# Optimization experiments

Hardware: AMD Instinct MI355X
Metric: run time of the kernel (lower is better)

The kernel has to match this reference:

```python
import jax, jax.numpy as jnp
import numpy as np

T, B, I, H, O = 256, 64, 512, 1024, 256


def setup_inputs() -> dict:
    key = jax.random.key(0)
    ks = jax.random.split(key, 7)
    s_ih = 1.0 / np.sqrt(H)
    return {
        "x": jax.random.normal(ks[0], (T, B, I), dtype=jnp.float32),
        "W_ih": jax.random.uniform(ks[1], (4 * H, I), dtype=jnp.float32, minval=-s_ih, maxval=s_ih),
        "W_hh": jax.random.uniform(ks[2], (4 * H, H), dtype=jnp.float32, minval=-s_ih, maxval=s_ih),
        "b_ih": jax.random.uniform(ks[3], (4 * H,), dtype=jnp.float32, minval=-s_ih, maxval=s_ih),
        "b_hh": jax.random.uniform(ks[4], (4 * H,), dtype=jnp.float32, minval=-s_ih, maxval=s_ih),
        "fc_W": jax.random.uniform(ks[5], (O, H), dtype=jnp.float32, minval=-s_ih, maxval=s_ih),
        "fc_b": jax.random.uniform(ks[6], (O,), dtype=jnp.float32, minval=-s_ih, maxval=s_ih),
    }


def _lstm(x, W_ih, W_hh, b_ih, b_hh):
    # x: (T, B, I) seq-first, as PyTorch default. Gate order: i, f, g, o.
    Bsz = x.shape[1]
    Hh = W_hh.shape[1]
    # precompute input projections for all time steps: (T, B, 4H)
    xz = jnp.einsum('tbi,gi->tbg', x, W_ih) + b_ih + b_hh

    def step(carry, xz_t):
        h, c = carry
        z = xz_t + h @ W_hh.T  # (B, 4H)
        i, f, g, o = jnp.split(z, 4, axis=-1)
        i = jax.nn.sigmoid(i)
        f = jax.nn.sigmoid(f)
        g = jnp.tanh(g)
        o = jax.nn.sigmoid(o)
        c = f * c + i * g
        h = o * jnp.tanh(c)
        return (h, c), h

    h0 = jnp.zeros((Bsz, Hh), dtype=x.dtype)
    c0 = jnp.zeros((Bsz, Hh), dtype=x.dtype)
    _, hs = jax.lax.scan(step, (h0, c0), xz)
    return hs  # (T, B, H)


def reference(x, W_ih, W_hh, b_ih, b_hh, fc_W, fc_b):
    out = _lstm(x, W_ih, W_hh, b_ih, b_hh)  # (T, B, H)
    # Faithful to original: out[:, -1, :] indexes the LAST BATCH element
    # (seq-first layout), giving (T, H), then fc -> (T, O).
    last = out[:, -1, :]
    return last @ fc_W.T + fc_b
```

## Files before the change

kernel.cpp:

```cpp
#include <hip/hip_runtime.h>
#include <hip/hip_bf16.h>
#include <stdint.h>

#define T_STEPS 256
#define BATCH   64
#define IN_DIM  512
#define HID     1024
#define OUT_DIM 256
#define G4      4096
#define SENT32  0x7FC07FC0u
#define SENT64  0x7FC07FC07FC07FC0ULL

__device__ __forceinline__ float bfbits2f(uint32_t b16) {
    return __uint_as_float(b16 << 16);
}
__device__ __forceinline__ uint32_t f2bfbits(float f) {
    uint32_t u = __float_as_uint(f);
    u += 0x7fffu + ((u >> 16) & 1u);
    return u >> 16;
}
__device__ __forceinline__ float fast_sigmoid(float x) {
    return 1.f / (1.f + __expf(-x));
}
__device__ __forceinline__ float fast_tanh(float x) {
    return 2.f / (1.f + __expf(-2.f * x)) - 1.f;
}
__device__ __forceinline__ bool any_sent(uint64_t v) {
    uint64_t x = v ^ SENT64;
    return (((x - 0x0001000100010001ULL) & ~x) & 0x8000800080008000ULL) != 0ULL;
}
__device__ __forceinline__ uint64_t poll_load(const uint64_t* p) {
    return __hip_atomic_load(p, __ATOMIC_RELAXED, __HIP_MEMORY_SCOPE_AGENT);
}

__global__ void init_sent(uint32_t* __restrict__ p, int n) {
    int i = blockIdx.x * 256 + threadIdx.x;
    if (i < n) p[i] = SENT32;
}

template<bool ABF16>
__global__ __launch_bounds__(256) void gemm_bt(
    const void* __restrict__ Av, long lda,
    const float* __restrict__ Bw, int ldb,
    const float* __restrict__ bias1,
    float* __restrict__ C, int ldc, int K)
{
    __shared__ float a_lds[64][68];
    __shared__ float w_lds[64][65];
    const int tid = threadIdx.x;
    const int m0 = blockIdx.y * 64, n0 = blockIdx.x * 64;
    const int kl = tid & 63, grp = tid >> 6;
    const int cc = tid & 31, r0 = (tid >> 5) * 8;

    float acc[16];
#pragma unroll
    for (int i = 0; i < 16; ++i) acc[i] = 0.f;

    for (int k0 = 0; k0 < K; k0 += 64) {
        __syncthreads();
#pragma unroll
        for (int i = 0; i < 16; ++i) {
            int r = grp + 4 * i;
            long ai = (long)(m0 + r) * lda + k0 + kl;
            float av = ABF16 ? bfbits2f(((const uint16_t*)Av)[ai])
                             : ((const float*)Av)[ai];
            a_lds[kl][r] = av;
            w_lds[kl][r] = Bw[(long)(n0 + r) * ldb + k0 + kl];
        }
        __syncthreads();
#pragma unroll 16
        for (int k = 0; k < 64; ++k) {
            float4 A0 = *(const float4*)&a_lds[k][r0];
            float4 A1 = *(const float4*)&a_lds[k][r0 + 4];
            float w0 = w_lds[k][cc], w1 = w_lds[k][cc + 32];
            float a[8] = {A0.x, A0.y, A0.z, A0.w, A1.x, A1.y, A1.z, A1.w};
#pragma unroll
            for (int i = 0; i < 8; ++i) {
                acc[i]     += a[i] * w0;
                acc[8 + i] += a[i] * w1;
            }
        }
    }
    float b0 = bias1[n0 + cc], b1 = bias1[n0 + cc + 32];
#pragma unroll
    for (int i = 0; i < 8; ++i) {
        C[(long)(m0 + r0 + i) * ldc + n0 + cc]      = acc[i]     + b0;
        C[(long)(m0 + r0 + i) * ldc + n0 + cc + 32] = acc[8 + i] + b1;
    }
}

#define GROWX(RR) ((long)((RR) >> 3) * HID + 8 * g + ((RR) & 7))

#define WINIT(I) { const int ch_ = ((I) + kpart) & 15; \
    w##I = *(const float4*)(W_hh + wbase + ch_ * 4); }

#define MACS(I) { const float4 hv_ = *(const float4*)(hb + hoff + (((I) + kpart) & 15) * 4); \
    a0 = fmaf(w##I.x, hv_.x, a0); a1 = fmaf(w##I.y, hv_.y, a1); \
    a2 = fmaf(w##I.z, hv_.z, a2); a3 = fmaf(w##I.w, hv_.w, a3); }

__global__ __launch_bounds__(512, 2) void lstm_rec(
    const float* __restrict__ W_hh,
    const float* __restrict__ x,
    const float* __restrict__ W_ih,
    const float* __restrict__ b_ih,
    const float* __restrict__ b_hh,
    uint64_t* __restrict__ h_all)
{
    __shared__ float h_lds[2][HID];
    __shared__ float xz_lds[32][T_STEPS + 1];
    __shared__ float z_lds[32];
    extern __shared__ float dyn_pad[];

    const int g   = blockIdx.x;
    const int tid = threadIdx.x;

    {
        const int wv = tid >> 6;
        const int ln = tid & 63;
        const int rr0 = 4 * wv;
        const long gr0 = GROWX(rr0), gr1 = GROWX(rr0 + 1),
                   gr2 = GROWX(rr0 + 2), gr3 = GROWX(rr0 + 3);
        const float4 p0a = *(const float4*)(W_ih + gr0 * IN_DIM + 8 * ln);
        const float4 p0b = *(const float4*)(W_ih + gr0 * IN_DIM + 8 * ln + 4);
        const float4 p1a = *(const float4*)(W_ih + gr1 * IN_DIM + 8 * ln);
        const float4 p1b = *(const float4*)(W_ih + gr1 * IN_DIM + 8 * ln + 4);
        const float4 p2a = *(const float4*)(W_ih + gr2 * IN_DIM + 8 * ln);
        const float4 p2b = *(const float4*)(W_ih + gr2 * IN_DIM + 8 * ln + 4);
        const float4 p3a = *(const float4*)(W_ih + gr3 * IN_DIM + 8 * ln);
        const float4 p3b = *(const float4*)(W_ih + gr3 * IN_DIM + 8 * ln + 4);
        const float bs0 = b_ih[gr0] + b_hh[gr0];
        const float bs1 = b_ih[gr1] + b_hh[gr1];
        const float bs2 = b_ih[gr2] + b_hh[gr2];
        const float bs3 = b_ih[gr3] + b_hh[gr3];
        for (int t = 0; t < T_STEPS; ++t) {
            const float* xp = x + ((long)t * BATCH + 63) * IN_DIM + 8 * ln;
            const float4 xa = *(const float4*)xp;
            const float4 xb = *(const float4*)(xp + 4);
            float s0 = xa.x*p0a.x + xa.y*p0a.y + xa.z*p0a.z + xa.w*p0a.w
                     + xb.x*p0b.x + xb.y*p0b.y + xb.z*p0b.z + xb.w*p0b.w;
            float s1 = xa.x*p1a.x + xa.y*p1a.y + xa.z*p1a.z + xa.w*p1a.w
                     + xb.x*p1b.x + xb.y*p1b.y + xb.z*p1b.z + xb.w*p1b.w;
            float s2 = xa.x*p2a.x + xa.y*p2a.y + xa.z*p2a.z + xa.w*p2a.w
                     + xb.x*p2b.x + xb.y*p2b.y + xb.z*p2b.z + xb.w*p2b.w;
            float s3 = xa.x*p3a.x + xa.y*p3a.y + xa.z*p3a.z + xa.w*p3a.w
                     + xb.x*p3b.x + xb.y*p3b.y + xb.z*p3b.z + xb.w*p3b.w;
#pragma unroll
            for (int d = 1; d < 64; d <<= 1) {
                s0 += __shfl_xor(s0, d, 64);
                s1 += __shfl_xor(s1, d, 64);
                s2 += __shfl_xor(s2, d, 64);
                s3 += __shfl_xor(s3, d, 64);
            }
            if (ln == 0) {
                xz_lds[rr0 + 0][t] = s0 + bs0;
                xz_lds[rr0 + 1][t] = s1 + bs1;
                xz_lds[rr0 + 2][t] = s2 + bs2;
                xz_lds[rr0 + 3][t] = s3 + bs3;
            }
        }
    }

    if (tid < 256) {
        float4 z4 = {0.f, 0.f, 0.f, 0.f};
        *(float4*)&h_lds[0][4 * tid] = z4;
    }

    const int kpart = tid & 15;
    const int row   = tid >> 4;
    const long grow  = GROWX(row);
    const long wbase = grow * HID + kpart * 64;
    const int  hoff  = kpart * 64;
    float4 w0, w1, w2, w3, w4, w5, w6, w7, w8, w9, w10, w11, w12, w13, w14, w15;
    WINIT(0)  WINIT(1)  WINIT(2)  WINIT(3)
    WINIT(4)  WINIT(5)  WINIT(6)  WINIT(7)
    WINIT(8)  WINIT(9)  WINIT(10) WINIT(11)
    WINIT(12) WINIT(13) WINIT(14) WINIT(15)

    __syncthreads();

    float c_state = 0.f;
    float xz_next = xz_lds[row][0];

    for (int t = 0; t < T_STEPS; ++t) {
        float* hb = h_lds[t & 1];
        if (t > 0 && tid < 128) {
            const uint64_t* src = h_all + (size_t)(t - 1) * 256 + 2 * tid;
            uint64_t v0 = poll_load(src), v1 = poll_load(src + 1);
            if (any_sent(v0) | any_sent(v1)) {
                uint64_t a0_ = poll_load(src), a1_ = poll_load(src + 1);
                uint64_t b0_ = poll_load(src), b1_ = poll_load(src + 1);
                for (;;) {
                    uint64_t c0_ = poll_load(src), c1_ = poll_load(src + 1);
                    if (!(any_sent(v0) | any_sent(v1))) break;
                    v0 = a0_; v1 = a1_;
                    a0_ = b0_; a1_ = b1_;
                    b0_ = c0_; b1_ = c1_;
                }
            }
            float4 f0 = { bfbits2f((uint32_t)( v0        & 0xFFFFu)),
                          bfbits2f((uint32_t)((v0 >> 16) & 0xFFFFu)),
                          bfbits2f((uint32_t)((v0 >> 32) & 0xFFFFu)),
                          bfbits2f((uint32_t)((v0 >> 48) & 0xFFFFu)) };
            float4 f1 = { bfbits2f((uint32_t)( v1        & 0xFFFFu)),
                          bfbits2f((uint32_t)((v1 >> 16) & 0xFFFFu)),
                          bfbits2f((uint32_t)((v1 >> 32) & 0xFFFFu)),
                          bfbits2f((uint32_t)((v1 >> 48) & 0xFFFFu)) };
            *(float4*)&hb[8 * tid]     = f0;
            *(float4*)&hb[8 * tid + 4] = f1;
        }
        __syncthreads();

        const float xz_cur = xz_next;
        const int tn = (t + 1 < T_STEPS) ? t + 1 : t;
        xz_next = xz_lds[row][tn];

        float a0 = 0.f, a1 = 0.f, a2 = 0.f, a3 = 0.f;
        MACS(0)  MACS(1)  MACS(2)  MACS(3)
        MACS(4)  MACS(5)  MACS(6)  MACS(7)
        MACS(8)  MACS(9)  MACS(10) MACS(11)
        MACS(12) MACS(13) MACS(14) MACS(15)
        float sum = (a0 + a1) + (a2 + a3);
        sum += __shfl_xor(sum, 1, 16);
        sum += __shfl_xor(sum, 2, 16);
        sum += __shfl_xor(sum, 4, 16);
        sum += __shfl_xor(sum, 8, 16);
        if (kpart == 0) z_lds[row] = sum + xz_cur;
        __syncthreads();

        if (tid < 8) {
            const float zi = z_lds[tid],      zf = z_lds[8 + tid];
            const float zg = z_lds[16 + tid], zo = z_lds[24 + tid];
            const float ii = fast_sigmoid(zi);
            const float ff = fast_sigmoid(zf);
            const float gg = fast_tanh(zg);
            const float oo = fast_sigmoid(zo);
            c_state = ff * c_state + ii * gg;
            const float h = oo * fast_tanh(c_state);
            uint32_t hbv = f2bfbits(h);
            uint32_t lo  = hbv | (__shfl_down(hbv, 1, 64) << 16);
            uint64_t A = (uint64_t)lo | ((uint64_t)__shfl(lo, 2, 64) << 32);
            uint64_t B = (uint64_t)__shfl(lo, 4, 64)
                       | ((uint64_t)__shfl(lo, 6, 64) << 32);
            if (tid == 0) {
                uint64_t* dst = h_all + (size_t)t * 256 + 2 * g;
                __hip_atomic_store(dst,     A, __ATOMIC_RELAXED, __HIP_MEMORY_SCOPE_AGENT);
                __hip_atomic_store(dst + 1, B, __ATOMIC_RELAXED, __HIP_MEMORY_SCOPE_AGENT);
            }
        }
    }
    (void)dyn_pad;
}

extern "C" void kernel_launch(void* const* d_in, const int* in_sizes, int n_in,
                              void* d_out, int out_size, void* d_ws, size_t ws_size,
                              hipStream_t stream) {
    const float* x    = (const float*)d_in[0];
    const float* W_ih = (const float*)d_in[1];
    const float* W_hh = (const float*)d_in[2];
    const float* b_ih = (const float*)d_in[3];
    const float* b_hh = (const float*)d_in[4];
    const float* fc_W = (const float*)d_in[5];
    const float* fc_b = (const float*)d_in[6];
    float* out = (float*)d_out;

    uint64_t* h_all = (uint64_t*)d_ws;

    init_sent<<<512, 256, 0, stream>>>((uint32_t*)h_all, T_STEPS * HID / 2);

    lstm_rec<<<128, 512, 41984, stream>>>(W_hh, x, W_ih, b_ih, b_hh, h_all);

    gemm_bt<true><<<dim3(OUT_DIM / 64, T_STEPS / 64), 256, 0, stream>>>(
        (const void*)h_all, HID, fc_W, HID, fc_b, out, OUT_DIM, HID);
}
```

Baseline: 1.142 ms.

## Split LSTM recurrence over 256 blocks with W_hh slices held in LDS

Doubles the number of persistent recurrence blocks from 128 to 256, each owning 4 hidden units (16 gate rows) instead of 8. Each block's W_hh slice moves from registers into padded shared memory, and every thread now polls one 64-bit h chunk per step. The aim is to halve per-block matmul work on the serial critical path and spread the work over more CUs. In exchange, every step now reads weights from LDS, and twice as many blocks must synchronise through global-memory polling, which adds sync traffic and latency.

```diff
diff --git a/kernel.cpp b/kernel.cpp
--- a/kernel.cpp
+++ b/kernel.cpp
@@ -10,6 +10,7 @@
 #define G4      4096
 #define SENT32  0x7FC07FC0u
 #define SENT64  0x7FC07FC07FC07FC0ULL
+#define WSTRIDE 1028
 
 __device__ __forceinline__ float bfbits2f(uint32_t b16) {
     return __uint_as_float(b16 << 16);
@@ -89,16 +90,9 @@
     }
 }
 
-#define GROWX(RR) ((long)((RR) >> 3) * HID + 8 * g + ((RR) & 7))
-
-#define WINIT(I) { const int ch_ = ((I) + kpart) & 15; \
-    w##I = *(const float4*)(W_hh + wbase + ch_ * 4); }
-
-#define MACS(I) { const float4 hv_ = *(const float4*)(hb + hoff + (((I) + kpart) & 15) * 4); \
-    a0 = fmaf(w##I.x, hv_.x, a0); a1 = fmaf(w##I.y, hv_.y, a1); \
-    a2 = fmaf(w##I.z, hv_.z, a2); a3 = fmaf(w##I.w, hv_.w, a3); }
-
-__global__ __launch_bounds__(512, 2) void lstm_rec(
+#define GROWX(RR) ((long)((RR) >> 2) * HID + 4 * g + ((RR) & 3))
+
+__global__ __launch_bounds__(256, 1) void lstm_rec(
     const float* __restrict__ W_hh,
     const float* __restrict__ x,
     const float* __restrict__ W_ih,
@@ -106,13 +100,25 @@
     const float* __restrict__ b_hh,
     uint64_t* __restrict__ h_all)
 {
+    __shared__ float W_lds[16][WSTRIDE];
     __shared__ float h_lds[2][HID];
-    __shared__ float xz_lds[32][T_STEPS + 1];
-    __shared__ float z_lds[32];
-    extern __shared__ float dyn_pad[];
+    __shared__ float xz_lds[16][T_STEPS + 1];
+    __shared__ float z_lds[16];
 
     const int g   = blockIdx.x;
     const int tid = threadIdx.x;
+    const int kpart = tid & 15;
+    const int row   = tid >> 4;
+    const long grow = GROWX(row);
+
+    {
+        const float* wsrc = W_hh + grow * HID;
+#pragma unroll
+        for (int i = 0; i < 16; ++i) {
+            const int col = kpart * 64 + ((i + kpart) & 15) * 4;
+            *(float4*)&W_lds[row][col] = *(const float4*)(wsrc + col);
+        }
+    }
 
     {
         const int wv = tid >> 6;
@@ -160,22 +166,10 @@
         }
     }
 
-    if (tid < 256) {
+    {
         float4 z4 = {0.f, 0.f, 0.f, 0.f};
         *(float4*)&h_lds[0][4 * tid] = z4;
     }
-
-    const int kpart = tid & 15;
-    const int row   = tid >> 4;
-    const long grow  = GROWX(row);
-    const long wbase = grow * HID + kpart * 64;
-    const int  hoff  = kpart * 64;
-    float4 w0, w1, w2, w3, w4, w5, w6, w7, w8, w9, w10, w11, w12, w13, w14, w15;
-    WINIT(0)  WINIT(1)  WINIT(2)  WINIT(3)
-    WINIT(4)  WINIT(5)  WINIT(6)  WINIT(7)
-    WINIT(8)  WINIT(9)  WINIT(10) WINIT(11)
-    WINIT(12) WINIT(13) WINIT(14) WINIT(15)
-
     __syncthreads();
 
     float c_state = 0.f;
@@ -183,42 +177,38 @@
 
     for (int t = 0; t < T_STEPS; ++t) {
         float* hb = h_lds[t & 1];
-        if (t > 0 && tid < 128) {
-            const uint64_t* src = h_all + (size_t)(t - 1) * 256 + 2 * tid;
-            uint64_t v0 = poll_load(src), v1 = poll_load(src + 1);
-            if (any_sent(v0) | any_sent(v1)) {
-                uint64_t a0_ = poll_load(src), a1_ = poll_load(src + 1);
-                uint64_t b0_ = poll_load(src), b1_ = poll_load(src + 1);
-                for (;;) {
-                    uint64_t c0_ = poll_load(src), c1_ = poll_load(src + 1);
-                    if (!(any_sent(v0) | any_sent(v1))) break;
-                    v0 = a0_; v1 = a1_;
-                    a0_ = b0_; a1_ = b1_;
-                    b0_ = c0_; b1_ = c1_;
-                }
-            }
-            float4 f0 = { bfbits2f((uint32_t)( v0        & 0xFFFFu)),
-                          bfbits2f((uint32_t)((v0 >> 16) & 0xFFFFu)),
-                          bfbits2f((uint32_t)((v0 >> 32) & 0xFFFFu)),
-                          bfbits2f((uint32_t)((v0 >> 48) & 0xFFFFu)) };
-            float4 f1 = { bfbits2f((uint32_t)( v1        & 0xFFFFu)),
-                          bfbits2f((uint32_t)((v1 >> 16) & 0xFFFFu)),
-                          bfbits2f((uint32_t)((v1 >> 32) & 0xFFFFu)),
-                          bfbits2f((uint32_t)((v1 >> 48) & 0xFFFFu)) };
-            *(float4*)&hb[8 * tid]     = f0;
-            *(float4*)&hb[8 * tid + 4] = f1;
-        }
-        __syncthreads();
+        if (t > 0) {
+            const uint64_t* src = h_all + (size_t)(t - 1) * 256 + tid;
+            uint64_t v  = poll_load(src);
+            uint64_t a_ = poll_load(src);
+            uint64_t b_ = poll_load(src);
+            while (any_sent(v)) {
+                v = a_; a_ = b_; b_ = poll_load(src);
+            }
+            float4 f0 = { bfbits2f((uint32_t)( v        & 0xFFFFu)),
+                          bfbits2f((uint32_t)((v >> 16) & 0xFFFFu)),
+                          bfbits2f((uint32_t)((v >> 32) & 0xFFFFu)),
+                          bfbits2f((uint32_t)((v >> 48) & 0xFFFFu)) };
+            *(float4*)&hb[4 * tid] = f0;
+        }
+        __syncthreads();
+        asm volatile("" ::: "memory");
 
         const float xz_cur = xz_next;
         const int tn = (t + 1 < T_STEPS) ? t + 1 : t;
         xz_next = xz_lds[row][tn];
 
         float a0 = 0.f, a1 = 0.f, a2 = 0.f, a3 = 0.f;
-        MACS(0)  MACS(1)  MACS(2)  MACS(3)
-        MACS(4)  MACS(5)  MACS(6)  MACS(7)
-        MACS(8)  MACS(9)  MACS(10) MACS(11)
-        MACS(12) MACS(13) MACS(14) MACS(15)
+#pragma unroll
+        for (int i = 0; i < 16; ++i) {
+            const int col = kpart * 64 + ((i + kpart) & 15) * 4;
+            const float4 wv4 = *(const float4*)&W_lds[row][col];
+            const float4 hv  = *(const float4*)&hb[col];
+            a0 = fmaf(wv4.x, hv.x, a0);
+            a1 = fmaf(wv4.y, hv.y, a1);
+            a2 = fmaf(wv4.z, hv.z, a2);
+            a3 = fmaf(wv4.w, hv.w, a3);
+        }
         float sum = (a0 + a1) + (a2 + a3);
         sum += __shfl_xor(sum, 1, 16);
         sum += __shfl_xor(sum, 2, 16);
@@ -227,9 +217,9 @@
         if (kpart == 0) z_lds[row] = sum + xz_cur;
         __syncthreads();
 
-        if (tid < 8) {
-            const float zi = z_lds[tid],      zf = z_lds[8 + tid];
-            const float zg = z_lds[16 + tid], zo = z_lds[24 + tid];
+        if (tid < 4) {
+            const float zi = z_lds[tid],     zf = z_lds[4 + tid];
+            const float zg = z_lds[8 + tid], zo = z_lds[12 + tid];
             const float ii = fast_sigmoid(zi);
             const float ff = fast_sigmoid(zf);
             const float gg = fast_tanh(zg);
@@ -238,17 +228,13 @@
             const float h = oo * fast_tanh(c_state);
             uint32_t hbv = f2bfbits(h);
             uint32_t lo  = hbv | (__shfl_down(hbv, 1, 64) << 16);
-            uint64_t A = (uint64_t)lo | ((uint64_t)__shfl(lo, 2, 64) << 32);
-            uint64_t B = (uint64_t)__shfl(lo, 4, 64)
-                       | ((uint64_t)__shfl(lo, 6, 64) << 32);
+            uint64_t A   = (uint64_t)lo | ((uint64_t)__shfl(lo, 2, 64) << 32);
             if (tid == 0) {
-                uint64_t* dst = h_all + (size_t)t * 256 + 2 * g;
-                __hip_atomic_store(dst,     A, __ATOMIC_RELAXED, __HIP_MEMORY_SCOPE_AGENT);
-                __hip_atomic_store(dst + 1, B, __ATOMIC_RELAXED, __HIP_MEMORY_SCOPE_AGENT);
-            }
-        }
-    }
-    (void)dyn_pad;
+                __hip_atomic_store(&h_all[(size_t)t * 256 + g], A,
+                                   __ATOMIC_RELAXED, __HIP_MEMORY_SCOPE_AGENT);
+            }
+        }
+    }
 }
 
 extern "C" void kernel_launch(void* const* d_in, const int* in_sizes, int n_in,
@@ -267,7 +253,7 @@
 
     init_sent<<<512, 256, 0, stream>>>((uint32_t*)h_all, T_STEPS * HID / 2);
 
-    lstm_rec<<<128, 512, 41984, stream>>>(W_hh, x, W_ih, b_ih, b_hh, h_all);
+    lstm_rec<<<256, 256, 0, stream>>>(W_hh, x, W_ih, b_ih, b_hh, h_all);
 
     gemm_bt<true><<<dim3(OUT_DIM / 64, T_STEPS / 64), 256, 0, stream>>>(
         (const void*)h_all, HID, fc_W, HID, fc_b, out, OUT_DIM, HID);
```

After: 1.163 ms. Within noise of the previous version (+1.8%).
